# Kernel tuning notes

Hardware: AMD Instinct MI355X
Metric: run time of the kernel (lower is better)

Reference implementation:

```python
import jax, jax.numpy as jnp
import numpy as np

B, N, K, T = 64, 32768, 128, 512
TMAX = 512  # number of discrete time bins (round(t*10) range)


def setup_inputs() -> dict:
    key = jax.random.key(0)
    k1, k2, k3, k4, k5, k6 = jax.random.split(key, 6)
    state = jax.random.normal(k1, (B, N, 4), dtype=jnp.float32)
    time_idx = jax.random.randint(k2, (B, N), 0, TMAX, dtype=jnp.int32)
    # unique_ids in [-1, K-1]; -1 marks clutter (invalid) measurements
    unique_ids = jax.random.randint(k3, (B, N), 0, K + 1, dtype=jnp.int32) - 1
    # trajectory states [B,K,T,5]: cols [x, y, vx, vy, t] with round(t*10) in 0..TMAX-1
    xy = jax.random.normal(k4, (B, K, T, 2), dtype=jnp.float32)
    vel = jax.random.normal(k5, (B, K, T, 2), dtype=jnp.float32)
    # per-(b,k) permutation of 0..T-1 -> unique times within each trajectory
    times = jnp.argsort(jax.random.uniform(k6, (B, K, T)), axis=-1).astype(jnp.float32)
    traj_states = jnp.concatenate([xy, vel, (times / 10.0)[..., None]], axis=-1)
    return {"state": state, "time_idx": time_idx, "unique_ids": unique_ids,
            "traj_states": traj_states}


def reference(state, time_idx, unique_ids, traj_states):
    xy = state[..., :2]                                   # [B,N,2]
    tvals = jnp.round(traj_states[..., 4] * 10.0).astype(jnp.int32)  # [B,K,T]
    traj_xy = traj_states[..., :2]                        # [B,K,T,2]
    # dense lookup table [B,K,TMAX,2]; default 0 matches torch.zeros_like(tgt)
    b_ix = jnp.arange(B)[:, None, None]
    k_ix = jnp.arange(K)[None, :, None]
    table = jnp.zeros((B, K, TMAX, 2), dtype=state.dtype)
    table = table.at[b_ix, k_ix, tvals].set(traj_xy, mode="drop")
    # gather tgt per measurement by (object id, time bin)
    obj = jnp.clip(unique_ids, 0, K - 1)
    tcl = jnp.clip(time_idx, 0, TMAX - 1)
    tgt = table[jnp.arange(B)[:, None], obj, tcl]         # [B,N,2]
    valid = unique_ids >= 0
    tgt = jnp.where(valid[..., None], tgt, 0.0)
    diff = jnp.abs(xy - tgt).sum(-1)                      # [B,N]
    vf = valid.astype(state.dtype)
    loss = (diff * vf).sum() / vf.sum()
    return loss
```

## Files before the change

kernel.cpp:

```cpp
#include <hip/hip_runtime.h>
#include <hip/hip_fp16.h>

constexpr int Bc = 64;
constexpr int Nc = 32768;
constexpr int Kc = 128;
constexpr int Tc = 512;
constexpr int TMAXc = 512;
constexpr int BK = Bc * Kc;

typedef float f32x4 __attribute__((ext_vector_type(4)));
typedef float f32x2 __attribute__((ext_vector_type(2)));

constexpr size_t TABLE_BYTES = (size_t)Bc * Kc * TMAXc * 4;
constexpr int NBLK1 = BK / 2;
constexpr int NBLK2 = 512;

__global__ __launch_bounds__(256) void build_table_k(
    const f32x4* __restrict__ traj4,
    uint2* __restrict__ table2)
{
    __shared__ __align__(16) float    stage[2 * Tc * 5];
    __shared__ __align__(8)  unsigned tbl[2 * TMAXc];

    const int j   = blockIdx.x;
    const int xcd = j & 7;
    const int s   = j >> 3;
    const int b   = ((s >> 6) << 3) | xcd;
    const int k2  = s & 63;
    const int bk0 = (b << 7) | (k2 << 1);

    const f32x4* src = traj4 + (size_t)bk0 * 640;
    #pragma unroll
    for (int r = 0; r < 5; ++r) {
        int t = threadIdx.x + r * 256;
        ((f32x4*)stage)[t] = __builtin_nontemporal_load(&src[t]);
    }
    __syncthreads();

    #pragma unroll
    for (int r = 0; r < 4; ++r) {
        int t = threadIdx.x + r * 256;
        float x  = stage[t * 5 + 0];
        float y  = stage[t * 5 + 1];
        float tv = stage[t * 5 + 4];
        int tau = __float2int_rn(tv * 10.0f);
        if ((unsigned)tau < (unsigned)TMAXc) {
            __half2 p = __floats2half2_rn(x, y);
            unsigned raw;
            __builtin_memcpy(&raw, &p, 4);
            tbl[((t >> 9) << 9) + tau] = raw;
        }
    }
    __syncthreads();

    uint2* dst = table2 + (size_t)bk0 * 256;
    #pragma unroll
    for (int r = 0; r < 2; ++r) {
        int t = threadIdx.x + r * 256;
        dst[t] = ((const uint2*)tbl)[t];
    }
}

__global__ __launch_bounds__(256) void gather_reduce_k(
    const f32x2*    __restrict__ state2,
    const int*      __restrict__ tidx,
    const int*      __restrict__ uid,
    const unsigned* __restrict__ table,
    float2*         __restrict__ partials)
{
    const int j     = blockIdx.x;
    const int xcd   = j & 7;
    const int s     = j >> 3;
    const int b     = ((s >> 3) << 3) | xcd;
    const int chunk = s & 7;
    const int base  = (b << 15) + (chunk << 12);
    const unsigned* tb = table + ((long long)b << 16);

    f32x2    sv[16];
    int      idv[16], tiv[16];
    unsigned tg[16];

    #pragma unroll
    for (int r = 0; r < 16; ++r) {
        int i = base + r * 256 + threadIdx.x;
        sv[r]  = __builtin_nontemporal_load(&state2[2 * (size_t)i]);
        idv[r] = __builtin_nontemporal_load(&uid[i]);
        tiv[r] = __builtin_nontemporal_load(&tidx[i]);
    }
    #pragma unroll
    for (int r = 0; r < 16; ++r) {
        int obj = min(max(idv[r], 0), Kc - 1);
        int tcl = min(max(tiv[r], 0), TMAXc - 1);
        tg[r] = tb[(obj << 9) + tcl];
    }
    float sum = 0.0f, cnt = 0.0f;
    #pragma unroll
    for (int r = 0; r < 16; ++r) {
        __half2 p;
        __builtin_memcpy(&p, &tg[r], 4);
        float tx = __low2float(p);
        float ty = __high2float(p);
        if (idv[r] >= 0) {
            sum += fabsf(sv[r].x - tx) + fabsf(sv[r].y - ty);
            cnt += 1.0f;
        }
    }

    #pragma unroll
    for (int off = 32; off > 0; off >>= 1) {
        sum += __shfl_down(sum, off, 64);
        cnt += __shfl_down(cnt, off, 64);
    }
    __shared__ float2 lds[4];
    int lane = threadIdx.x & 63;
    int w    = threadIdx.x >> 6;
    if (lane == 0) lds[w] = make_float2(sum, cnt);
    __syncthreads();
    if (threadIdx.x == 0) {
        float s2 = 0.0f, c2 = 0.0f;
        #pragma unroll
        for (int q = 0; q < 4; ++q) { s2 += lds[q].x; c2 += lds[q].y; }
        partials[j] = make_float2(s2, c2);
    }
}

__global__ __launch_bounds__(512) void final_reduce_k(
    const float2* __restrict__ partials, float* __restrict__ out)
{
    float s, c;
    {
        float2 p = partials[threadIdx.x];
        s = p.x; c = p.y;
    }
    #pragma unroll
    for (int off = 32; off > 0; off >>= 1) {
        s += __shfl_down(s, off, 64);
        c += __shfl_down(c, off, 64);
    }
    __shared__ float2 lds[8];
    int lane = threadIdx.x & 63;
    int w    = threadIdx.x >> 6;
    if (lane == 0) lds[w] = make_float2(s, c);
    __syncthreads();
    if (threadIdx.x == 0) {
        float s2 = 0.0f, c2 = 0.0f;
        #pragma unroll
        for (int q = 0; q < 8; ++q) { s2 += lds[q].x; c2 += lds[q].y; }
        out[0] = s2 / c2;
    }
}

extern "C" void kernel_launch(void* const* d_in, const int* in_sizes, int n_in,
                              void* d_out, int out_size, void* d_ws, size_t ws_size,
                              hipStream_t stream) {
    const f32x2* state2 = (const f32x2*)d_in[0];
    const int*   tidx   = (const int*)  d_in[1];
    const int*   uid    = (const int*)  d_in[2];
    const f32x4* traj4  = (const f32x4*)d_in[3];
    float* out = (float*)d_out;

    unsigned* table    = (unsigned*)d_ws;
    float2*   partials = (float2*)((char*)d_ws + TABLE_BYTES);

    build_table_k  <<<NBLK1, 256, 0, stream>>>(traj4, (uint2*)table);
    gather_reduce_k<<<NBLK2, 256, 0, stream>>>(state2, tidx, uid, table, partials);
    final_reduce_k <<<1, 512, 0, stream>>>(partials, out);
}
```

Baseline: 38.91 us.

## Fuse final reduction into gather kernel via last-block atomic counter and double grid

Removes the separate final_reduce kernel launch: each gather block writes its partial, bumps an atomic counter (reset inside build_table_k), and the last block to arrive reduces all partials and writes the loss. The gather grid also doubles to 1024 blocks, each handling 8 elements per thread instead of 16, for more parallelism. This trades one launch plus its inter-kernel gap for an atomic and threadfence per block, with less memory-level parallelism per thread.

```diff
diff --git a/kernel.cpp b/kernel.cpp
--- a/kernel.cpp
+++ b/kernel.cpp
@@ -11,18 +11,20 @@
 typedef float f32x4 __attribute__((ext_vector_type(4)));
 typedef float f32x2 __attribute__((ext_vector_type(2)));
 
-constexpr size_t TABLE_BYTES = (size_t)Bc * Kc * TMAXc * 4;
+constexpr size_t TABLE_BYTES = (size_t)BK * TMAXc * 4;
 constexpr int NBLK1 = BK / 2;
-constexpr int NBLK2 = 512;
+constexpr int NBLK2 = 1024;
 
 __global__ __launch_bounds__(256) void build_table_k(
     const f32x4* __restrict__ traj4,
-    uint2* __restrict__ table2)
+    uint2* __restrict__ table2,
+    unsigned* __restrict__ counter)
 {
     __shared__ __align__(16) float    stage[2 * Tc * 5];
     __shared__ __align__(8)  unsigned tbl[2 * TMAXc];
 
     const int j   = blockIdx.x;
+    if (j == 0 && threadIdx.x == 0) *counter = 0u;
     const int xcd = j & 7;
     const int s   = j >> 3;
     const int b   = ((s >> 6) << 3) | xcd;
@@ -66,36 +68,38 @@
     const int*      __restrict__ tidx,
     const int*      __restrict__ uid,
     const unsigned* __restrict__ table,
-    float2*         __restrict__ partials)
+    float2*         __restrict__ partials,
+    unsigned*       __restrict__ counter,
+    float*          __restrict__ out)
 {
     const int j     = blockIdx.x;
     const int xcd   = j & 7;
     const int s     = j >> 3;
-    const int b     = ((s >> 3) << 3) | xcd;
-    const int chunk = s & 7;
-    const int base  = (b << 15) + (chunk << 12);
+    const int b     = ((s >> 4) << 3) | xcd;
+    const int chunk = s & 15;
+    const int base  = (b << 15) + (chunk << 11);
     const unsigned* tb = table + ((long long)b << 16);
 
-    f32x2    sv[16];
-    int      idv[16], tiv[16];
-    unsigned tg[16];
+    f32x2    sv[8];
+    int      idv[8], tiv[8];
+    unsigned tg[8];
 
     #pragma unroll
-    for (int r = 0; r < 16; ++r) {
+    for (int r = 0; r < 8; ++r) {
         int i = base + r * 256 + threadIdx.x;
         sv[r]  = __builtin_nontemporal_load(&state2[2 * (size_t)i]);
         idv[r] = __builtin_nontemporal_load(&uid[i]);
         tiv[r] = __builtin_nontemporal_load(&tidx[i]);
     }
     #pragma unroll
-    for (int r = 0; r < 16; ++r) {
+    for (int r = 0; r < 8; ++r) {
         int obj = min(max(idv[r], 0), Kc - 1);
         int tcl = min(max(tiv[r], 0), TMAXc - 1);
         tg[r] = tb[(obj << 9) + tcl];
     }
     float sum = 0.0f, cnt = 0.0f;
     #pragma unroll
-    for (int r = 0; r < 16; ++r) {
+    for (int r = 0; r < 8; ++r) {
         __half2 p;
         __builtin_memcpy(&p, &tg[r], 4);
         float tx = __low2float(p);
@@ -111,42 +115,45 @@
         sum += __shfl_down(sum, off, 64);
         cnt += __shfl_down(cnt, off, 64);
     }
-    __shared__ float2 lds[4];
-    int lane = threadIdx.x & 63;
-    int w    = threadIdx.x >> 6;
-    if (lane == 0) lds[w] = make_float2(sum, cnt);
+    __shared__ float2 lred[4];
+    const int lane = threadIdx.x & 63;
+    const int w    = threadIdx.x >> 6;
+    if (lane == 0) lred[w] = make_float2(sum, cnt);
     __syncthreads();
+
+    __shared__ unsigned is_last;
     if (threadIdx.x == 0) {
         float s2 = 0.0f, c2 = 0.0f;
         #pragma unroll
-        for (int q = 0; q < 4; ++q) { s2 += lds[q].x; c2 += lds[q].y; }
+        for (int q = 0; q < 4; ++q) { s2 += lred[q].x; c2 += lred[q].y; }
         partials[j] = make_float2(s2, c2);
+        __threadfence();
+        unsigned old = atomicAdd(counter, 1u);
+        is_last = (old == (unsigned)(NBLK2 - 1)) ? 1u : 0u;
     }
-}
+    __syncthreads();
+    if (!is_last) return;
 
-__global__ __launch_bounds__(512) void final_reduce_k(
-    const float2* __restrict__ partials, float* __restrict__ out)
-{
-    float s, c;
-    {
-        float2 p = partials[threadIdx.x];
-        s = p.x; c = p.y;
+    __threadfence();
+    float s2 = 0.0f, c2 = 0.0f;
+    #pragma unroll
+    for (int r = 0; r < 4; ++r) {
+        float2 p = partials[threadIdx.x + r * 256];
+        s2 += p.x; c2 += p.y;
     }
     #pragma unroll
     for (int off = 32; off > 0; off >>= 1) {
-        s += __shfl_down(s, off, 64);
-        c += __shfl_down(c, off, 64);
+        s2 += __shfl_down(s2, off, 64);
+        c2 += __shfl_down(c2, off, 64);
     }
-    __shared__ float2 lds[8];
-    int lane = threadIdx.x & 63;
-    int w    = threadIdx.x >> 6;
-    if (lane == 0) lds[w] = make_float2(s, c);
+    __shared__ float2 lred2[4];
+    if (lane == 0) lred2[w] = make_float2(s2, c2);
     __syncthreads();
     if (threadIdx.x == 0) {
-        float s2 = 0.0f, c2 = 0.0f;
+        float s3 = 0.0f, c3 = 0.0f;
         #pragma unroll
-        for (int q = 0; q < 8; ++q) { s2 += lds[q].x; c2 += lds[q].y; }
-        out[0] = s2 / c2;
+        for (int q = 0; q < 4; ++q) { s3 += lred2[q].x; c3 += lred2[q].y; }
+        out[0] = s3 / c3;
     }
 }
 
@@ -161,8 +168,9 @@
 
     unsigned* table    = (unsigned*)d_ws;
     float2*   partials = (float2*)((char*)d_ws + TABLE_BYTES);
+    unsigned* counter  = (unsigned*)((char*)d_ws + TABLE_BYTES + NBLK2 * 8);
 
-    build_table_k  <<<NBLK1, 256, 0, stream>>>(traj4, (uint2*)table);
-    gather_reduce_k<<<NBLK2, 256, 0, stream>>>(state2, tidx, uid, table, partials);
-    final_reduce_k <<<1, 512, 0, stream>>>(partials, out);
+    build_table_k  <<<NBLK1, 256, 0, stream>>>(traj4, (uint2*)table, counter);
+    gather_reduce_k<<<NBLK2, 256, 0, stream>>>(state2, tidx, uid, table,
+                                               partials, counter, out);
 }
```

Result: slower. 79.74 us (+104.9%).

## Split table build and gather by batch halves to overlap phases

Applied to the files above, without the earlier changes.

The table build and gather-reduce are split into batch halves across three launches. A mixed kernel builds the second half's table while gathering from the first half, so the two memory-bound phases overlap within one launch and reduce the tail and idle time between them. This adds one extra kernel launch and a branchy kernel whose two roles use different amounts of LDS, which can hurt occupancy.

```diff
diff --git a/kernel.cpp b/kernel.cpp
--- a/kernel.cpp
+++ b/kernel.cpp
@@ -11,21 +11,20 @@
 typedef float f32x4 __attribute__((ext_vector_type(4)));
 typedef float f32x2 __attribute__((ext_vector_type(2)));
 
-constexpr size_t TABLE_BYTES = (size_t)Bc * Kc * TMAXc * 4;
-constexpr int NBLK1 = BK / 2;
-constexpr int NBLK2 = 512;
-
-__global__ __launch_bounds__(256) void build_table_k(
-    const f32x4* __restrict__ traj4,
-    uint2* __restrict__ table2)
+constexpr size_t TABLE_BYTES = (size_t)BK * TMAXc * 4;
+
+constexpr int P1_HALF_BLOCKS = 2048;
+constexpr int P2_HALF_BLOCKS = 256;
+
+__device__ __forceinline__ void p1_role(int j, int boff,
+    const f32x4* __restrict__ traj4, uint2* __restrict__ table2)
 {
     __shared__ __align__(16) float    stage[2 * Tc * 5];
     __shared__ __align__(8)  unsigned tbl[2 * TMAXc];
 
-    const int j   = blockIdx.x;
     const int xcd = j & 7;
     const int s   = j >> 3;
-    const int b   = ((s >> 6) << 3) | xcd;
+    const int b   = boff + (((s >> 6) << 3) | xcd);
     const int k2  = s & 63;
     const int bk0 = (b << 7) | (k2 << 1);
 
@@ -61,17 +60,16 @@
     }
 }
 
-__global__ __launch_bounds__(256) void gather_reduce_k(
+__device__ __forceinline__ void p2_role(int jj, int boff,
     const f32x2*    __restrict__ state2,
     const int*      __restrict__ tidx,
     const int*      __restrict__ uid,
     const unsigned* __restrict__ table,
-    float2*         __restrict__ partials)
-{
-    const int j     = blockIdx.x;
-    const int xcd   = j & 7;
-    const int s     = j >> 3;
-    const int b     = ((s >> 3) << 3) | xcd;
+    float2*         __restrict__ partials, int pbase_idx)
+{
+    const int xcd   = jj & 7;
+    const int s     = jj >> 3;
+    const int b     = boff + (((s >> 3) << 3) | xcd);
     const int chunk = s & 7;
     const int base  = (b << 15) + (chunk << 12);
     const unsigned* tb = table + ((long long)b << 16);
@@ -111,17 +109,49 @@
         sum += __shfl_down(sum, off, 64);
         cnt += __shfl_down(cnt, off, 64);
     }
-    __shared__ float2 lds[4];
-    int lane = threadIdx.x & 63;
-    int w    = threadIdx.x >> 6;
-    if (lane == 0) lds[w] = make_float2(sum, cnt);
+    __shared__ float2 lred[4];
+    const int lane = threadIdx.x & 63;
+    const int w    = threadIdx.x >> 6;
+    if (lane == 0) lred[w] = make_float2(sum, cnt);
     __syncthreads();
     if (threadIdx.x == 0) {
         float s2 = 0.0f, c2 = 0.0f;
         #pragma unroll
-        for (int q = 0; q < 4; ++q) { s2 += lds[q].x; c2 += lds[q].y; }
-        partials[j] = make_float2(s2, c2);
-    }
+        for (int q = 0; q < 4; ++q) { s2 += lred[q].x; c2 += lred[q].y; }
+        partials[pbase_idx + jj] = make_float2(s2, c2);
+    }
+}
+
+__global__ __launch_bounds__(256) void build_half_k(
+    const f32x4* __restrict__ traj4, uint2* __restrict__ table2)
+{
+    p1_role(blockIdx.x, 0, traj4, table2);
+}
+
+__global__ __launch_bounds__(256) void mixed_k(
+    const f32x4* __restrict__ traj4, uint2* __restrict__ table2,
+    const f32x2* __restrict__ state2,
+    const int*   __restrict__ tidx,
+    const int*   __restrict__ uid,
+    float2*      __restrict__ partials)
+{
+    if (blockIdx.x < P1_HALF_BLOCKS) {
+        p1_role(blockIdx.x, 32, traj4, table2);
+    } else {
+        p2_role(blockIdx.x - P1_HALF_BLOCKS, 0, state2, tidx, uid,
+                (const unsigned*)table2, partials, 0);
+    }
+}
+
+__global__ __launch_bounds__(256) void gather_half_k(
+    const f32x2* __restrict__ state2,
+    const int*   __restrict__ tidx,
+    const int*   __restrict__ uid,
+    const uint2* __restrict__ table2,
+    float2*      __restrict__ partials)
+{
+    p2_role(blockIdx.x, 32, state2, tidx, uid,
+            (const unsigned*)table2, partials, P2_HALF_BLOCKS);
 }
 
 __global__ __launch_bounds__(512) void final_reduce_k(
@@ -159,10 +189,13 @@
     const f32x4* traj4  = (const f32x4*)d_in[3];
     float* out = (float*)d_out;
 
-    unsigned* table    = (unsigned*)d_ws;
-    float2*   partials = (float2*)((char*)d_ws + TABLE_BYTES);
-
-    build_table_k  <<<NBLK1, 256, 0, stream>>>(traj4, (uint2*)table);
-    gather_reduce_k<<<NBLK2, 256, 0, stream>>>(state2, tidx, uid, table, partials);
-    final_reduce_k <<<1, 512, 0, stream>>>(partials, out);
-}
+    uint2*  table    = (uint2*)d_ws;
+    float2* partials = (float2*)((char*)d_ws + TABLE_BYTES);
+
+    build_half_k <<<P1_HALF_BLOCKS, 256, 0, stream>>>(traj4, table);
+    mixed_k      <<<P1_HALF_BLOCKS + P2_HALF_BLOCKS, 256, 0, stream>>>(
+                     traj4, table, state2, tidx, uid, partials);
+    gather_half_k<<<P2_HALF_BLOCKS, 256, 0, stream>>>(state2, tidx, uid,
+                                                      table, partials);
+    final_reduce_k<<<1, 512, 0, stream>>>(partials, out);
+}
```

After: 47.49 us. 1.22x slower.
